# Optimization experiments

Hardware: AMD Instinct MI355X
Metric: run time of the kernel (lower is better)

Reference implementation:

```python
import jax, jax.numpy as jnp
import numpy as np
from jax import lax

NB, NC, NH, NW, NT, NCLASS = 128, 256, 8, 128, 64, 128
NHID = NC // 2  # bidirectional LSTM hidden per direction


def _lengths():
    rng = np.random.default_rng(0)
    lengths = rng.integers(NT // 2, NT + 1, size=NB)
    lengths[0] = NT  # ensure nsteps == nT
    return lengths


def setup_inputs() -> dict:
    key = jax.random.key(0)
    ks = jax.random.split(key, 20)
    s = 0.05
    lengths = _lengths()
    d = {}
    d['feature'] = jax.random.normal(ks[0], (NB, NC, NH, NW), jnp.float32)
    d['A'] = jax.random.uniform(ks[1], (NB, NT, NH, NW), jnp.float32, 1e-3, 1.0)
    d['text'] = jax.random.randint(ks[2], (NB, NT), 0, NCLASS)
    d['text_length'] = jnp.asarray(lengths, jnp.int32)
    d['pack_b'] = jnp.asarray(np.repeat(np.arange(NB), lengths), jnp.int32)
    d['pack_t'] = jnp.asarray(np.concatenate([np.arange(l) for l in lengths]), jnp.int32)
    d['emb'] = jax.random.normal(ks[3], (NCLASS, NC), jnp.float32)  # char_embeddings ~ randn
    # pre_lstm (PyTorch gate order i,f,g,o), forward and backward directions
    d['Wih_f'] = s * jax.random.normal(ks[4], (4 * NHID, NC), jnp.float32)
    d['Whh_f'] = s * jax.random.normal(ks[5], (4 * NHID, NHID), jnp.float32)
    d['bih_f'] = s * jax.random.normal(ks[6], (4 * NHID,), jnp.float32)
    d['bhh_f'] = s * jax.random.normal(ks[7], (4 * NHID,), jnp.float32)
    d['Wih_b'] = s * jax.random.normal(ks[8], (4 * NHID, NC), jnp.float32)
    d['Whh_b'] = s * jax.random.normal(ks[9], (4 * NHID, NHID), jnp.float32)
    d['bih_b'] = s * jax.random.normal(ks[10], (4 * NHID,), jnp.float32)
    d['bhh_b'] = s * jax.random.normal(ks[11], (4 * NHID,), jnp.float32)
    # GRUCell (PyTorch gate order r,z,n): input 2*NC, hidden NC
    d['Wih_g'] = s * jax.random.normal(ks[12], (3 * NC, 2 * NC), jnp.float32)
    d['Whh_g'] = s * jax.random.normal(ks[13], (3 * NC, NC), jnp.float32)
    d['bih_g'] = s * jax.random.normal(ks[14], (3 * NC,), jnp.float32)
    d['bhh_g'] = s * jax.random.normal(ks[15], (3 * NC,), jnp.float32)
    # generator Linear NC -> NCLASS (dropout treated as identity for determinism)
    d['Wgen'] = s * jax.random.normal(ks[16], (NCLASS, NC), jnp.float32)
    d['bgen'] = s * jax.random.normal(ks[17], (NCLASS,), jnp.float32)
    return d


def _lstm_dir(x, Wih, Whh, bih, bhh, reverse):
    nB = x.shape[1]
    h0 = jnp.zeros((nB, Whh.shape[1]), x.dtype)
    b = bih + bhh

    def step(carry, xt):
        h, c = carry
        g = xt @ Wih.T + h @ Whh.T + b
        i, f, gg, o = jnp.split(g, 4, axis=-1)
        c = jax.nn.sigmoid(f) * c + jax.nn.sigmoid(i) * jnp.tanh(gg)
        h = jax.nn.sigmoid(o) * jnp.tanh(c)
        return (h, c), h

    _, ys = lax.scan(step, (h0, h0), x, reverse=reverse)
    return ys


def reference(feature, A, text, text_length, pack_b, pack_t, emb, Wih_f, Whh_f, bih_f, bhh_f, Wih_b, Whh_b, bih_b, bhh_b, Wih_g, Whh_g, bih_g, bhh_g, Wgen, bgen):
    # normalize attention maps over spatial dims
    A_norm = A / A.reshape(NB, NT, -1).sum(-1)[:, :, None, None]  # [nB,nT,nH,nW]
    # attention-pooled features, fused (avoids [nB,nT,nC,nH,nW] blowup): -> [nT,nB,nC]
    C = jnp.einsum('bchw,bthw->tbc', feature, A_norm)
    # bidirectional LSTM (dropout after LSTM treated as identity)
    Cf = _lstm_dir(C, Wih_f, Whh_f, bih_f, bhh_f, False)
    Cb = _lstm_dir(C, Wih_b, Whh_b, bih_b, bhh_b, True)
    Cl = jnp.concatenate([Cf, Cb], axis=-1)  # [nT,nB,nC]
    # teacher forcing (current_epoch=0): prev_emb[0]=emb[0], prev_emb[t]=emb[text[:,t-1]]
    prev = jnp.concatenate([jnp.broadcast_to(emb[0][None, None, :], (1, NB, NC)), emb[text[:, :NT - 1].T]], axis=0)
    xs = jnp.concatenate([Cl, prev], axis=-1)  # [nT,nB,2*nC]
    h0 = jnp.zeros((NB, NC), C.dtype)

    def gstep(h, xt):
        gx = xt @ Wih_g.T + bih_g
        gh = h @ Whh_g.T + bhh_g
        rx, zx, nx = jnp.split(gx, 3, axis=-1)
        rh, zh, nh = jnp.split(gh, 3, axis=-1)
        r = jax.nn.sigmoid(rx + rh)
        z = jax.nn.sigmoid(zx + zh)
        n = jnp.tanh(nx + r * nh)
        h = (1.0 - z) * n + z * h
        return h, h

    _, hs = lax.scan(gstep, h0, xs)  # [nT,nB,nC]
    logits = hs @ Wgen.T + bgen  # [nT,nB,nclass]
    # ragged packing: concat per-sample valid steps (vectorized gather)
    out_res = logits[pack_t, pack_b]  # [lenText,nclass]
    out_attns = A_norm[pack_b, pack_t]  # [lenText,nH,nW]
    return out_res, out_attns
```

## Files before the change

kernel.cpp:

```cpp
#include <hip/hip_runtime.h>
#include <cstdint>
#include <cstddef>

#define NBATCH 128
#define NCH    256
#define NHW    1024
#define NTIME  64
#define NCLS   128

typedef _Float16 f16_t;
typedef _Float16 f16x8 __attribute__((ext_vector_type(8)));
typedef _Float16 half2_t __attribute__((ext_vector_type(2)));
typedef short bf16x8 __attribute__((ext_vector_type(8)));
typedef short bf16x4 __attribute__((ext_vector_type(4)));
typedef float f32x4 __attribute__((ext_vector_type(4)));
typedef unsigned short ushort_t;

#if defined(__has_builtin)
#  if __has_builtin(__builtin_amdgcn_fdot2)
#    define HAS_FDOT2 1
#  endif
#endif
#ifndef HAS_FDOT2
#  define HAS_FDOT2 0
#endif

__device__ __forceinline__ float dot2acc(half2_t a, half2_t b, float c){
#if HAS_FDOT2
  return __builtin_amdgcn_fdot2(a, b, c, false);
#else
  return c + (float)a.x*(float)b.x + (float)a.y*(float)b.y;
#endif
}
__device__ __forceinline__ half2_t pack2(float x, float y){
  half2_t p; p.x = (_Float16)x; p.y = (_Float16)y; return p;
}
#define BCH(x) __builtin_bit_cast(half2_t, (x))
__device__ __forceinline__ ushort_t f2bf(float x){
  unsigned u = __builtin_bit_cast(unsigned, x);
  unsigned r = (u + 0x7FFFu + ((u>>16)&1u)) >> 16;
  return (ushort_t)r;
}
__device__ __forceinline__ float sig_(float x){
  x = fminf(30.f, fmaxf(-30.f, x));
  return 1.f/(1.f+__expf(-x));
}
__device__ __forceinline__ float tanh_(float x){
  x = fminf(15.f, fmaxf(-15.f, x));
  float e = __expf(2.f*x);
  return (e-1.f)/(e+1.f);
}

__global__ __launch_bounds__(256) void k_prep(
    const float* __restrict__ Wih_f, const float* __restrict__ Wih_b,
    const float* __restrict__ Wih_g, const float* __restrict__ Wgen,
    const float* __restrict__ Whh_f, const float* __restrict__ Whh_b,
    const float* __restrict__ Whh_g, const float* __restrict__ emb,
    ushort_t* __restrict__ Wf_bf, ushort_t* __restrict__ Wb_bf,
    ushort_t* __restrict__ Wg_bf, ushort_t* __restrict__ Wgen_bf,
    f16_t* __restrict__ Whf_h, f16_t* __restrict__ Whb_h, f16_t* __restrict__ Whg_h,
    ushort_t* __restrict__ emb_bf){
  int i = blockIdx.x*256 + threadIdx.x;
  if (i < 131072){ Wf_bf[i] = f2bf(Wih_f[i]); return; }
  i -= 131072;
  if (i < 131072){ Wb_bf[i] = f2bf(Wih_b[i]); return; }
  i -= 131072;
  if (i < 393216){ Wg_bf[i] = f2bf(Wih_g[i]); return; }
  i -= 393216;
  if (i < 32768){ Wgen_bf[i] = f2bf(Wgen[i]); return; }
  i -= 32768;
  if (i < 65536){ Whf_h[i] = (f16_t)Whh_f[i]; return; }
  i -= 65536;
  if (i < 65536){ Whb_h[i] = (f16_t)Whh_b[i]; return; }
  i -= 65536;
  if (i < 196608){ Whg_h[i] = (f16_t)Whh_g[i]; return; }
  i -= 196608;
  emb_bf[i] = f2bf(emb[i]);
}

__global__ __launch_bounds__(256) void k_pool_mfma(const float* __restrict__ feat, const float* __restrict__ A,
    float* __restrict__ S, ushort_t* __restrict__ Cbf){
  __shared__ ushort_t As_[64*40];
  __shared__ ushort_t Fs_[128*40];
  __shared__ float sinvs[64];
  __shared__ float psum[512];
  int b = blockIdx.x >> 1, ch = blockIdx.x & 1, c0 = ch*128;
  int tid = threadIdx.x, wave = tid>>6, lane = tid&63;
  f32x4 acc[4][2] = {};
  int lr = lane & 15, lk = (lane>>4)*8;
  float sA0 = 0.f, sA1 = 0.f;
  for (int k0=0;k0<NHW;k0+=32){
    __syncthreads();
    #pragma unroll
    for (int i=0;i<2;i++){
      int c = tid + i*256, r = c>>3, kq = c&7;
      float4 v = *(const float4*)(A + ((size_t)(b*64+r))*NHW + k0 + kq*4);
      float sv = v.x+v.y+v.z+v.w;
      if (i==0) sA0 += sv; else sA1 += sv;
      bf16x4 p; p[0]=(short)f2bf(v.x); p[1]=(short)f2bf(v.y); p[2]=(short)f2bf(v.z); p[3]=(short)f2bf(v.w);
      *(bf16x4*)&As_[r*40 + kq*4] = p;
    }
    #pragma unroll
    for (int i=0;i<4;i++){
      int c = tid + i*256, r = c>>3, kq = c&7;
      float4 v = *(const float4*)(feat + ((size_t)(b*256+c0+r))*NHW + k0 + kq*4);
      bf16x4 p; p[0]=(short)f2bf(v.x); p[1]=(short)f2bf(v.y); p[2]=(short)f2bf(v.z); p[3]=(short)f2bf(v.w);
      *(bf16x4*)&Fs_[r*40 + kq*4] = p;
    }
    __syncthreads();
    bf16x8 af[4], bg[2];
    #pragma unroll
    for (int m=0;m<4;m++) af[m] = *(const bf16x8*)&As_[(m*16 + lr)*40 + lk];
    #pragma unroll
    for (int n=0;n<2;n++) bg[n] = *(const bf16x8*)&Fs_[(wave*32 + n*16 + lr)*40 + lk];
    #pragma unroll
    for (int m=0;m<4;m++)
      #pragma unroll
      for (int n=0;n<2;n++)
        acc[m][n] = __builtin_amdgcn_mfma_f32_16x16x32_bf16(af[m], bg[n], acc[m][n], 0, 0, 0);
  }
  psum[tid] = sA0;
  psum[tid+256] = sA1;
  __syncthreads();
  if (tid < 64){
    float s = 0.f;
    #pragma unroll
    for (int j=0;j<8;j++) s += psum[tid*8 + j];
    sinvs[tid] = 1.f / s;
    if (ch == 0) S[b*64 + tid] = s;
  }
  __syncthreads();
  #pragma unroll
  for (int m=0;m<4;m++)
    #pragma unroll
    for (int n=0;n<2;n++)
      #pragma unroll
      for (int j=0;j<4;j++){
        int t = m*16 + (lane>>4)*4 + j;
        int c = c0 + wave*32 + n*16 + lr;
        Cbf[((size_t)t*NBATCH + b)*NCH + c] = f2bf(acc[m][n][j] * sinvs[t]);
      }
}

__global__ __launch_bounds__(256) void k_gemm_bf(const ushort_t* __restrict__ X, const ushort_t* __restrict__ W,
    const float* __restrict__ ba, const float* __restrict__ bb, float* __restrict__ out, int N, int K){
  __shared__ ushort_t Xs[128*40];
  __shared__ ushort_t Ws[128*40];
  int n0 = blockIdx.x*128, m0 = blockIdx.y*128;
  int tid = threadIdx.x, wave = tid>>6, lane = tid&63;
  int wr = wave>>1, wc = wave&1;
  int lr = lane & 15, lk = (lane>>4)*8;
  f32x4 acc[4][4] = {};
  for (int k0=0;k0<K;k0+=32){
    __syncthreads();
    #pragma unroll
    for (int i=0;i<2;i++){
      int c = tid + i*256, r = c>>2, kb = c&3;
      *(bf16x8*)&Xs[r*40 + kb*8] = *(const bf16x8*)(X + (size_t)(m0+r)*K + k0 + kb*8);
      *(bf16x8*)&Ws[r*40 + kb*8] = *(const bf16x8*)(W + (size_t)(n0+r)*K + k0 + kb*8);
    }
    __syncthreads();
    bf16x8 af[4], bg[4];
    #pragma unroll
    for (int m=0;m<4;m++) af[m] = *(const bf16x8*)&Xs[(wr*64 + m*16 + lr)*40 + lk];
    #pragma unroll
    for (int n=0;n<4;n++) bg[n] = *(const bf16x8*)&Ws[(wc*64 + n*16 + lr)*40 + lk];
    #pragma unroll
    for (int m=0;m<4;m++)
      #pragma unroll
      for (int n=0;n<4;n++)
        acc[m][n] = __builtin_amdgcn_mfma_f32_16x16x32_bf16(af[m], bg[n], acc[m][n], 0, 0, 0);
  }
  float bsv[4];
  #pragma unroll
  for (int n=0;n<4;n++){
    int col = n0 + wc*64 + n*16 + lr;
    bsv[n] = ba[col] + (bb ? bb[col] : 0.f);
  }
  #pragma unroll
  for (int m=0;m<4;m++)
    #pragma unroll
    for (int n=0;n<4;n++)
      #pragma unroll
      for (int j=0;j<4;j++){
        int row = m0 + wr*64 + m*16 + (lane>>4)*4 + j;
        int col = n0 + wc*64 + n*16 + lr;
        out[(size_t)row*N + col] = acc[m][n][j] + bsv[n];
      }
}

__global__ __launch_bounds__(256) void k_gemm_gx(const ushort_t* __restrict__ Clbf,
    const ushort_t* __restrict__ emb_bf, const int* __restrict__ text,
    const ushort_t* __restrict__ W, const float* __restrict__ ba,
    float* __restrict__ out){
  __shared__ ushort_t Xs[128*40];
  __shared__ ushort_t Ws[128*40];
  __shared__ int clsL[128];
  const int N = 768, K = 512;
  int n0 = blockIdx.x*128, m0 = blockIdx.y*128;
  int tid = threadIdx.x, wave = tid>>6, lane = tid&63;
  int wr = wave>>1, wc = wave&1;
  int lr = lane & 15, lk = (lane>>4)*8;
  if (tid < 128){
    int m = m0 + tid, t = m>>7, b = m&127;
    clsL[tid] = (t==0) ? 0 : text[b*64 + (t-1)];
  }
  f32x4 acc[4][4] = {};
  __syncthreads();
  for (int k0=0;k0<K;k0+=32){
    __syncthreads();
    #pragma unroll
    for (int i=0;i<2;i++){
      int c = tid + i*256, r = c>>2, kb = c&3;
      int col = k0 + kb*8;
      bf16x8 xv;
      if (col < 256) xv = *(const bf16x8*)(Clbf + (size_t)(m0+r)*NCH + col);
      else           xv = *(const bf16x8*)(emb_bf + (size_t)clsL[r]*NCH + (col-256));
      *(bf16x8*)&Xs[r*40 + kb*8] = xv;
      *(bf16x8*)&Ws[r*40 + kb*8] = *(const bf16x8*)(W + (size_t)(n0+r)*K + k0 + kb*8);
    }
    __syncthreads();
    bf16x8 af[4], bg[4];
    #pragma unroll
    for (int m=0;m<4;m++) af[m] = *(const bf16x8*)&Xs[(wr*64 + m*16 + lr)*40 + lk];
    #pragma unroll
    for (int n=0;n<4;n++) bg[n] = *(const bf16x8*)&Ws[(wc*64 + n*16 + lr)*40 + lk];
    #pragma unroll
    for (int m=0;m<4;m++)
      #pragma unroll
      for (int n=0;n<4;n++)
        acc[m][n] = __builtin_amdgcn_mfma_f32_16x16x32_bf16(af[m], bg[n], acc[m][n], 0, 0, 0);
  }
  float bsv[4];
  #pragma unroll
  for (int n=0;n<4;n++) bsv[n] = ba[n0 + wc*64 + n*16 + lr];
  #pragma unroll
  for (int m=0;m<4;m++)
    #pragma unroll
    for (int n=0;n<4;n++)
      #pragma unroll
      for (int j=0;j<4;j++){
        int row = m0 + wr*64 + m*16 + (lane>>4)*4 + j;
        int col = n0 + wc*64 + n*16 + lr;
        out[(size_t)row*N + col] = acc[m][n][j] + bsv[n];
      }
}

__global__ __launch_bounds__(256) void k_attns(const float* __restrict__ A, const float* __restrict__ S,
    const int* __restrict__ pack_b, const int* __restrict__ pack_t, float* __restrict__ outA){
  int i = blockIdx.x;
  int b = pack_b[i], t = pack_t[i];
  float is = 1.f / S[b*64 + t];
  float4 v = ((const float4*)(A + ((size_t)(b*64+t))*NHW))[threadIdx.x];
  v.x*=is; v.y*=is; v.z*=is; v.w*=is;
  ((float4*)(outA + (size_t)i*NHW))[threadIdx.x] = v;
}

__global__ __launch_bounds__(512) void k_lstm_ldsT(const float* __restrict__ Gf, const float* __restrict__ Gb,
    const f16_t* __restrict__ Whf, const f16_t* __restrict__ Whb, ushort_t* __restrict__ Clbf){
  extern __shared__ char smem[];
  int2*  Wt2   = (int2*)smem;
  float* h32   = (float*)(smem + 131072);
  float* gates = (float*)(smem + 131072 + 512);
  int b = blockIdx.x & 127, dir = blockIdx.x >> 7;
  const f16_t* W = dir ? Whb : Whf;
  const float* G = dir ? Gb : Gf;
  int g = threadIdx.x, lane = g & 63;
  {
    const int2* wr = (const int2*)(W + (size_t)g*128);
    #pragma unroll
    for (int p2=0;p2<32;p2++) Wt2[p2*512 + g] = wr[p2];
  }
  if (g < 128) h32[g] = 0.f;
  float c = 0.f;
  __syncthreads();
  #pragma unroll 1
  for (int t=0;t<NTIME;t++){
    int tt = dir ? (NTIME-1-t) : t;
    float gv = G[((size_t)tt*NBATCH + b)*512 + g];
    float2 hp2 = *(const float2*)(h32 + 2*lane);
    int hpk = __builtin_bit_cast(int, pack2(hp2.x, hp2.y));
    float a0=0.f, a1=0.f, a2=0.f, a3=0.f;
    #pragma unroll
    for (int p2=0;p2<32;p2+=2){
      int2 w0 = Wt2[p2*512 + g];
      int2 w1 = Wt2[(p2+1)*512 + g];
      int h0 = __builtin_amdgcn_readlane(hpk, 2*p2);
      int h1 = __builtin_amdgcn_readlane(hpk, 2*p2+1);
      int h2 = __builtin_amdgcn_readlane(hpk, 2*p2+2);
      int h3 = __builtin_amdgcn_readlane(hpk, 2*p2+3);
      a0 = dot2acc(BCH(w0.x), BCH(h0), a0);
      a1 = dot2acc(BCH(w0.y), BCH(h1), a1);
      a2 = dot2acc(BCH(w1.x), BCH(h2), a2);
      a3 = dot2acc(BCH(w1.y), BCH(h3), a3);
    }
    gates[g] = gv + a0+a1+a2+a3;
    __syncthreads();
    if (g < 128){
      float gi=gates[g], gf=gates[128+g], gg=gates[256+g], go=gates[384+g];
      c = sig_(gf)*c + sig_(gi)*tanh_(gg);
      float h = sig_(go)*tanh_(c);
      h32[g] = h;
      Clbf[((size_t)tt*NBATCH + b)*NCH + dir*128 + g] = f2bf(h);
    }
    __syncthreads();
  }
}

__global__ __launch_bounds__(512, 1) void k_gru(const float* __restrict__ gx,
    const float* __restrict__ Whh_g, const float* __restrict__ bhh_g, ushort_t* __restrict__ hsbf){
  int b = blockIdx.x, t0 = threadIdx.x, lane = t0 & 63, w = t0 >> 6;
  half2_t wpA[64], wpB[64], wpC[64];
  int pidxA, pidxB, pidxC;
  int hfbA, hfbB, hfbC;

#define LOADW(WP, PIDX, HFB, S) do { \
    int c = w*3 + (S); \
    int hf = (c >= 12) ? 1 : 0; \
    int row = (c - hf*12)*64 + lane; \
    PIDX = hf*768 + row; \
    HFB  = __builtin_amdgcn_readfirstlane(hf*32); \
    const float4* wr = (const float4*)(Whh_g + (size_t)row*256 + hf*128); \
    _Pragma("unroll") \
    for (int j=0;j<32;j++){ \
      float4 v = wr[j]; \
      WP[2*j]   = pack2(v.x, v.y); \
      WP[2*j+1] = pack2(v.z, v.w); \
    } \
  } while(0)

  LOADW(wpA, pidxA, hfbA, 0);
  LOADW(wpB, pidxB, hfbB, 1);
  LOADW(wpC, pidxC, hfbC, 2);
#undef LOADW

  __shared__ float h32[256];
  __shared__ float partLds[1536];
  __shared__ float bhL[768];
  if (t0 < 256) h32[t0] = 0.f;
  bhL[t0] = bhh_g[t0];
  if (t0 < 256) bhL[512+t0] = bhh_g[512+t0];
  float hprev = 0.f;
  __syncthreads();
  #pragma unroll 1
  for (int t=0;t<NTIME;t++){
    float gxr=0.f, gxz=0.f, gxn=0.f;
    if (t0 < 256){
      const float* gxp = gx + ((size_t)t*NBATCH + b)*768;
      gxr = gxp[t0]; gxz = gxp[256+t0]; gxn = gxp[512+t0];
    }
    float4 hq = *(const float4*)(h32 + 4*lane);
    int hpk0 = __builtin_bit_cast(int, pack2(hq.x, hq.y));
    int hpk1 = __builtin_bit_cast(int, pack2(hq.z, hq.w));

#define DOTASK(WP, PIDX, HFB) do { \
    float a0=0.f, a1=0.f, a2=0.f, a3=0.f; \
    _Pragma("unroll") \
    for (int jj=0;jj<64;jj+=2){ \
      int hv0 = __builtin_amdgcn_readlane(hpk0, HFB + (jj>>1)); \
      int hv1 = __builtin_amdgcn_readlane(hpk1, HFB + (jj>>1)); \
      if ((jj>>1)&1){ \
        a2 = dot2acc(WP[jj],   __builtin_bit_cast(half2_t, hv0), a2); \
        a3 = dot2acc(WP[jj+1], __builtin_bit_cast(half2_t, hv1), a3); \
      } else { \
        a0 = dot2acc(WP[jj],   __builtin_bit_cast(half2_t, hv0), a0); \
        a1 = dot2acc(WP[jj+1], __builtin_bit_cast(half2_t, hv1), a1); \
      } \
    } \
    partLds[PIDX] = a0+a1+a2+a3; \
  } while(0)

    DOTASK(wpA, pidxA, hfbA);
    DOTASK(wpB, pidxB, hfbB);
    DOTASK(wpC, pidxC, hfbC);
#undef DOTASK

    __syncthreads();
    if (t0 < 256){
      float rh = bhL[t0]     + partLds[t0]     + partLds[768+t0];
      float zh = bhL[256+t0] + partLds[256+t0] + partLds[1024+t0];
      float nh = bhL[512+t0] + partLds[512+t0] + partLds[1280+t0];
      float r = sig_(gxr + rh);
      float z = sig_(gxz + zh);
      float n = tanh_(gxn + r*nh);
      float h = (1.f-z)*n + z*hprev;
      hprev = h;
      h32[t0] = h;
      hsbf[((size_t)t*NBATCH + b)*NCH + t0] = f2bf(h);
    }
    __syncthreads();
  }
}

__global__ __launch_bounds__(256) void k_logits_mfma(const ushort_t* __restrict__ hsbf,
    const int* __restrict__ pack_t, const int* __restrict__ pack_b,
    const ushort_t* __restrict__ Wbf, const float* __restrict__ bias,
    float* __restrict__ out, int L){
  __shared__ ushort_t Xs[64*40];
  __shared__ ushort_t Ws[128*40];
  __shared__ int rrow[64];
  int m0 = blockIdx.x*64;
  int tid = threadIdx.x, wave = tid>>6, lane = tid&63;
  int lr = lane & 15, lk = (lane>>4)*8;
  if (tid < 64){
    int m = m0 + tid;
    int pt = (m<L) ? pack_t[m] : 0;
    int pb = (m<L) ? pack_b[m] : 0;
    rrow[tid] = pt*NBATCH + pb;
  }
  f32x4 acc[4][2] = {};
  for (int k0=0;k0<NCH;k0+=32){
    __syncthreads();
    {
      int r = tid>>2, kb = tid&3;
      *(bf16x8*)&Xs[r*40 + kb*8] = *(const bf16x8*)(hsbf + (size_t)rrow[r]*NCH + k0 + kb*8);
    }
    #pragma unroll
    for (int i=0;i<2;i++){
      int c = tid + i*256, r = c>>2, kb = c&3;
      *(bf16x8*)&Ws[r*40 + kb*8] = *(const bf16x8*)(Wbf + (size_t)r*NCH + k0 + kb*8);
    }
    __syncthreads();
    bf16x8 af[4], bg[2];
    #pragma unroll
    for (int m=0;m<4;m++) af[m] = *(const bf16x8*)&Xs[(m*16 + lr)*40 + lk];
    #pragma unroll
    for (int n=0;n<2;n++) bg[n] = *(const bf16x8*)&Ws[(wave*32 + n*16 + lr)*40 + lk];
    #pragma unroll
    for (int m=0;m<4;m++)
      #pragma unroll
      for (int n=0;n<2;n++)
        acc[m][n] = __builtin_amdgcn_mfma_f32_16x16x32_bf16(af[m], bg[n], acc[m][n], 0, 0, 0);
  }
  #pragma unroll
  for (int m=0;m<4;m++)
    #pragma unroll
    for (int n=0;n<2;n++)
      #pragma unroll
      for (int j=0;j<4;j++){
        int row = m0 + m*16 + (lane>>4)*4 + j;
        int col = wave*32 + n*16 + lr;
        if (row < L) out[(size_t)row*NCLS + col] = acc[m][n][j] + bias[col];
      }
}

extern "C" void kernel_launch(void* const* d_in, const int* in_sizes, int n_in,
                              void* d_out, int out_size, void* d_ws, size_t ws_size,
                              hipStream_t stream) {
  const float* feature = (const float*)d_in[0];
  const float* A       = (const float*)d_in[1];
  const int*   text    = (const int*)d_in[2];
  const int*   pack_b  = (const int*)d_in[4];
  const int*   pack_t  = (const int*)d_in[5];
  const float* emb     = (const float*)d_in[6];
  const float* Wih_f   = (const float*)d_in[7];
  const float* Whh_f   = (const float*)d_in[8];
  const float* bih_f   = (const float*)d_in[9];
  const float* bhh_f   = (const float*)d_in[10];
  const float* Wih_b   = (const float*)d_in[11];
  const float* Whh_b   = (const float*)d_in[12];
  const float* bih_b   = (const float*)d_in[13];
  const float* bhh_b   = (const float*)d_in[14];
  const float* Wih_g   = (const float*)d_in[15];
  const float* Whh_g   = (const float*)d_in[16];
  const float* bih_g   = (const float*)d_in[17];
  const float* bhh_g   = (const float*)d_in[18];
  const float* Wgen    = (const float*)d_in[19];
  const float* bgen    = (const float*)d_in[20];
  int L = in_sizes[4];

  char* ws = (char*)d_ws;
  const size_t KB = 1024, MB = 1u<<20;
  float*    S       = (float*)(ws + 0);
  ushort_t* Wf_bf   = (ushort_t*)(ws + 1*MB);
  ushort_t* Wb_bf   = (ushort_t*)(ws + 1*MB + 256*KB);
  ushort_t* Wg_bf   = (ushort_t*)(ws + 1*MB + 512*KB);
  ushort_t* Wgen_bf = (ushort_t*)(ws + 2*MB + 256*KB);
  f16_t*    Whf_h   = (f16_t*)(ws + 2*MB + 512*KB);
  f16_t*    Whb_h   = (f16_t*)(ws + 2*MB + 640*KB);
  f16_t*    Whg_h   = (f16_t*)(ws + 2*MB + 768*KB);
  ushort_t* emb_bf  = (ushort_t*)(ws + 3*MB + 256*KB);
  ushort_t* Cbf     = (ushort_t*)(ws + 4*MB);
  ushort_t* Clbf    = (ushort_t*)(ws + 8*MB);
  ushort_t* hsbf    = (ushort_t*)(ws + 12*MB);
  float*    Gf      = (float*)(ws + 16*MB);
  float*    Gb      = (float*)(ws + 32*MB);
  float*    gx      = (float*)(ws + 24*MB);

  float* out_res   = (float*)d_out;
  float* out_attns = out_res + (size_t)L*NCLS;

  const int LSTM_SMEM = 131072 + 512 + 2048;
  (void)hipFuncSetAttribute((const void*)k_lstm_ldsT,
                            hipFuncAttributeMaxDynamicSharedMemorySize, LSTM_SMEM);

  k_prep<<<4096, 256, 0, stream>>>(Wih_f, Wih_b, Wih_g, Wgen, Whh_f, Whh_b, Whh_g, emb,
                                   Wf_bf, Wb_bf, Wg_bf, Wgen_bf, Whf_h, Whb_h, Whg_h, emb_bf);
  k_pool_mfma<<<256, 256, 0, stream>>>(feature, A, S, Cbf);
  k_attns<<<L, 256, 0, stream>>>(A, S, pack_b, pack_t, out_attns);
  k_gemm_bf<<<dim3(4,64), 256, 0, stream>>>(Cbf, Wf_bf, bih_f, bhh_f, Gf, 512, 256);
  k_gemm_bf<<<dim3(4,64), 256, 0, stream>>>(Cbf, Wb_bf, bih_b, bhh_b, Gb, 512, 256);
  k_lstm_ldsT<<<256, 512, LSTM_SMEM, stream>>>(Gf, Gb, Whf_h, Whb_h, Clbf);
  k_gemm_gx<<<dim3(6,64), 256, 0, stream>>>(Clbf, emb_bf, text, Wg_bf, bih_g, gx);
  k_gru<<<128, 512, 0, stream>>>(gx, Whh_g, bhh_g, hsbf);
  k_logits_mfma<<<(L+63)/64, 256, 0, stream>>>(hsbf, pack_t, pack_b, Wgen_bf, bgen, out_res, L);
}
```

Before: 324.8 us.

## Replicate recurrent cell update per wave to drop second barrier in LSTM and GRU

```diff
diff --git a/kernel.cpp b/kernel.cpp
--- a/kernel.cpp
+++ b/kernel.cpp
@@ -260,26 +260,24 @@
     const f16_t* __restrict__ Whf, const f16_t* __restrict__ Whb, ushort_t* __restrict__ Clbf){
   extern __shared__ char smem[];
   int2*  Wt2   = (int2*)smem;
-  float* h32   = (float*)(smem + 131072);
-  float* gates = (float*)(smem + 131072 + 512);
+  float* gates = (float*)(smem + 131072);
   int b = blockIdx.x & 127, dir = blockIdx.x >> 7;
   const f16_t* W = dir ? Whb : Whf;
   const float* G = dir ? Gb : Gf;
-  int g = threadIdx.x, lane = g & 63;
+  int g = threadIdx.x, lane = g & 63, w = g >> 6;
   {
     const int2* wr = (const int2*)(W + (size_t)g*128);
     #pragma unroll
     for (int p2=0;p2<32;p2++) Wt2[p2*512 + g] = wr[p2];
   }
-  if (g < 128) h32[g] = 0.f;
-  float c = 0.f;
+  int hpk = 0;
+  float c0s = 0.f, c1s = 0.f;
+  int buf = 0;
   __syncthreads();
   #pragma unroll 1
   for (int t=0;t<NTIME;t++){
     int tt = dir ? (NTIME-1-t) : t;
     float gv = G[((size_t)tt*NBATCH + b)*512 + g];
-    float2 hp2 = *(const float2*)(h32 + 2*lane);
-    int hpk = __builtin_bit_cast(int, pack2(hp2.x, hp2.y));
     float a0=0.f, a1=0.f, a2=0.f, a3=0.f;
     #pragma unroll
     for (int p2=0;p2<32;p2+=2){
@@ -294,16 +292,25 @@
       a2 = dot2acc(BCH(w1.x), BCH(h2), a2);
       a3 = dot2acc(BCH(w1.y), BCH(h3), a3);
     }
-    gates[g] = gv + a0+a1+a2+a3;
-    __syncthreads();
-    if (g < 128){
-      float gi=gates[g], gf=gates[128+g], gg=gates[256+g], go=gates[384+g];
-      c = sig_(gf)*c + sig_(gi)*tanh_(gg);
-      float h = sig_(go)*tanh_(c);
-      h32[g] = h;
-      Clbf[((size_t)tt*NBATCH + b)*NCH + dir*128 + g] = f2bf(h);
-    }
-    __syncthreads();
+    gates[buf*512 + g] = gv + a0+a1+a2+a3;
+    __syncthreads();
+    {
+      const float* GT = gates + buf*512;
+      float2 gi = *(const float2*)(GT + 2*lane);
+      float2 gf = *(const float2*)(GT + 128 + 2*lane);
+      float2 gg = *(const float2*)(GT + 256 + 2*lane);
+      float2 go = *(const float2*)(GT + 384 + 2*lane);
+      c0s = sig_(gf.x)*c0s + sig_(gi.x)*tanh_(gg.x);
+      float h0 = sig_(go.x)*tanh_(c0s);
+      c1s = sig_(gf.y)*c1s + sig_(gi.y)*tanh_(gg.y);
+      float h1 = sig_(go.y)*tanh_(c1s);
+      hpk = __builtin_bit_cast(int, pack2(h0, h1));
+      if (w == 0){
+        ushort2 o; o.x = f2bf(h0); o.y = f2bf(h1);
+        *(ushort2*)(Clbf + ((size_t)tt*NBATCH + b)*NCH + dir*128 + 2*lane) = o;
+      }
+    }
+    buf ^= 1;
   }
 }
 
@@ -334,24 +341,17 @@
   LOADW(wpC, pidxC, hfbC, 2);
 #undef LOADW
 
-  __shared__ float h32[256];
-  __shared__ float partLds[1536];
-  __shared__ float bhL[768];
-  if (t0 < 256) h32[t0] = 0.f;
-  bhL[t0] = bhh_g[t0];
-  if (t0 < 256) bhL[512+t0] = bhh_g[512+t0];
-  float hprev = 0.f;
+  __shared__ float partLds[2*1536];
+  float4 bR = *(const float4*)(bhh_g + 4*lane);
+  float4 bZ = *(const float4*)(bhh_g + 256 + 4*lane);
+  float4 bN = *(const float4*)(bhh_g + 512 + 4*lane);
+  float hp0=0.f, hp1=0.f, hp2=0.f, hp3=0.f;
+  int hpk0 = 0, hpk1 = 0;
+  int buf = 0;
   __syncthreads();
   #pragma unroll 1
   for (int t=0;t<NTIME;t++){
-    float gxr=0.f, gxz=0.f, gxn=0.f;
-    if (t0 < 256){
-      const float* gxp = gx + ((size_t)t*NBATCH + b)*768;
-      gxr = gxp[t0]; gxz = gxp[256+t0]; gxn = gxp[512+t0];
-    }
-    float4 hq = *(const float4*)(h32 + 4*lane);
-    int hpk0 = __builtin_bit_cast(int, pack2(hq.x, hq.y));
-    int hpk1 = __builtin_bit_cast(int, pack2(hq.z, hq.w));
+    float* P = partLds + buf*1536;
 
 #define DOTASK(WP, PIDX, HFB) do { \
     float a0=0.f, a1=0.f, a2=0.f, a3=0.f; \
@@ -367,7 +367,7 @@
         a1 = dot2acc(WP[jj+1], __builtin_bit_cast(half2_t, hv1), a1); \
       } \
     } \
-    partLds[PIDX] = a0+a1+a2+a3; \
+    P[PIDX] = a0+a1+a2+a3; \
   } while(0)
 
     DOTASK(wpA, pidxA, hfbA);
@@ -376,19 +376,38 @@
 #undef DOTASK
 
     __syncthreads();
-    if (t0 < 256){
-      float rh = bhL[t0]     + partLds[t0]     + partLds[768+t0];
-      float zh = bhL[256+t0] + partLds[256+t0] + partLds[1024+t0];
-      float nh = bhL[512+t0] + partLds[512+t0] + partLds[1280+t0];
-      float r = sig_(gxr + rh);
-      float z = sig_(gxz + zh);
-      float n = tanh_(gxn + r*nh);
-      float h = (1.f-z)*n + z*hprev;
-      hprev = h;
-      h32[t0] = h;
-      hsbf[((size_t)t*NBATCH + b)*NCH + t0] = f2bf(h);
-    }
-    __syncthreads();
+    {
+      float4 rA = *(const float4*)(P + 4*lane);
+      float4 rB = *(const float4*)(P + 768 + 4*lane);
+      float4 zA = *(const float4*)(P + 256 + 4*lane);
+      float4 zB = *(const float4*)(P + 1024 + 4*lane);
+      float4 nA = *(const float4*)(P + 512 + 4*lane);
+      float4 nB = *(const float4*)(P + 1280 + 4*lane);
+      const float* gxp = gx + ((size_t)t*NBATCH + b)*768;
+      float4 gR = *(const float4*)(gxp + 4*lane);
+      float4 gZ = *(const float4*)(gxp + 256 + 4*lane);
+      float4 gN = *(const float4*)(gxp + 512 + 4*lane);
+      float h[4];
+      #pragma unroll
+      for (int j=0;j<4;j++){
+        float rh = ((const float*)&bR)[j] + ((const float*)&rA)[j] + ((const float*)&rB)[j];
+        float zh = ((const float*)&bZ)[j] + ((const float*)&zA)[j] + ((const float*)&zB)[j];
+        float nh = ((const float*)&bN)[j] + ((const float*)&nA)[j] + ((const float*)&nB)[j];
+        float r = sig_(((const float*)&gR)[j] + rh);
+        float z = sig_(((const float*)&gZ)[j] + zh);
+        float n = tanh_(((const float*)&gN)[j] + r*nh);
+        float hp = (j==0)?hp0:(j==1)?hp1:(j==2)?hp2:hp3;
+        h[j] = (1.f - z)*n + z*hp;
+      }
+      hp0=h[0]; hp1=h[1]; hp2=h[2]; hp3=h[3];
+      hpk0 = __builtin_bit_cast(int, pack2(h[0], h[1]));
+      hpk1 = __builtin_bit_cast(int, pack2(h[2], h[3]));
+      if (w == 0){
+        ushort4 o; o.x=f2bf(h[0]); o.y=f2bf(h[1]); o.z=f2bf(h[2]); o.w=f2bf(h[3]);
+        *(ushort4*)(hsbf + ((size_t)t*NBATCH + b)*NCH + 4*lane) = o;
+      }
+    }
+    buf ^= 1;
   }
 }
 
@@ -490,7 +509,7 @@
   float* out_res   = (float*)d_out;
   float* out_attns = out_res + (size_t)L*NCLS;
 
-  const int LSTM_SMEM = 131072 + 512 + 2048;
+  const int LSTM_SMEM = 131072 + 2*512*4;
   (void)hipFuncSetAttribute((const void*)k_lstm_ldsT,
                             hipFuncAttributeMaxDynamicSharedMemorySize, LSTM_SMEM);
 
```

Result: slower. 388.9 us (+19.7%).

## Split GRU recurrent matvec across 1024 threads with four-way K split

Applied to the files above, without the earlier changes.

```diff
diff --git a/kernel.cpp b/kernel.cpp
--- a/kernel.cpp
+++ b/kernel.cpp
@@ -307,39 +307,32 @@
   }
 }
 
-__global__ __launch_bounds__(512, 1) void k_gru(const float* __restrict__ gx,
+__global__ __launch_bounds__(1024) void k_gru(const float* __restrict__ gx,
     const float* __restrict__ Whh_g, const float* __restrict__ bhh_g, ushort_t* __restrict__ hsbf){
   int b = blockIdx.x, t0 = threadIdx.x, lane = t0 & 63, w = t0 >> 6;
-  half2_t wpA[64], wpB[64], wpC[64];
-  int pidxA, pidxB, pidxC;
-  int hfbA, hfbB, hfbC;
-
-#define LOADW(WP, PIDX, HFB, S) do { \
-    int c = w*3 + (S); \
-    int hf = (c >= 12) ? 1 : 0; \
-    int row = (c - hf*12)*64 + lane; \
-    PIDX = hf*768 + row; \
-    HFB  = __builtin_amdgcn_readfirstlane(hf*32); \
-    const float4* wr = (const float4*)(Whh_g + (size_t)row*256 + hf*128); \
-    _Pragma("unroll") \
-    for (int j=0;j<32;j++){ \
-      float4 v = wr[j]; \
-      WP[2*j]   = pack2(v.x, v.y); \
-      WP[2*j+1] = pack2(v.z, v.w); \
-    } \
-  } while(0)
-
-  LOADW(wpA, pidxA, hfbA, 0);
-  LOADW(wpB, pidxB, hfbB, 1);
-  LOADW(wpC, pidxC, hfbC, 2);
-#undef LOADW
-
+  half2_t wp[3][32];
+  int pidx[3];
+  int q16[3];
+  #pragma unroll
+  for (int s=0;s<3;s++){
+    int c = w*3 + s;
+    int q = c/12, rg = c - q*12;
+    int row = rg*64 + lane;
+    pidx[s] = q*768 + row;
+    q16[s]  = __builtin_amdgcn_readfirstlane(q*16);
+    const float4* wr = (const float4*)(Whh_g + (size_t)row*256 + q*64);
+    #pragma unroll
+    for (int j=0;j<16;j++){
+      float4 v = wr[j];
+      wp[s][2*j]   = pack2(v.x, v.y);
+      wp[s][2*j+1] = pack2(v.z, v.w);
+    }
+  }
   __shared__ float h32[256];
-  __shared__ float partLds[1536];
+  __shared__ float partLds[3072];
   __shared__ float bhL[768];
   if (t0 < 256) h32[t0] = 0.f;
-  bhL[t0] = bhh_g[t0];
-  if (t0 < 256) bhL[512+t0] = bhh_g[512+t0];
+  if (t0 < 768) bhL[t0] = bhh_g[t0];
   float hprev = 0.f;
   __syncthreads();
   #pragma unroll 1
@@ -352,34 +345,27 @@
     float4 hq = *(const float4*)(h32 + 4*lane);
     int hpk0 = __builtin_bit_cast(int, pack2(hq.x, hq.y));
     int hpk1 = __builtin_bit_cast(int, pack2(hq.z, hq.w));
-
-#define DOTASK(WP, PIDX, HFB) do { \
-    float a0=0.f, a1=0.f, a2=0.f, a3=0.f; \
-    _Pragma("unroll") \
-    for (int jj=0;jj<64;jj+=2){ \
-      int hv0 = __builtin_amdgcn_readlane(hpk0, HFB + (jj>>1)); \
-      int hv1 = __builtin_amdgcn_readlane(hpk1, HFB + (jj>>1)); \
-      if ((jj>>1)&1){ \
-        a2 = dot2acc(WP[jj],   __builtin_bit_cast(half2_t, hv0), a2); \
-        a3 = dot2acc(WP[jj+1], __builtin_bit_cast(half2_t, hv1), a3); \
-      } else { \
-        a0 = dot2acc(WP[jj],   __builtin_bit_cast(half2_t, hv0), a0); \
-        a1 = dot2acc(WP[jj+1], __builtin_bit_cast(half2_t, hv1), a1); \
-      } \
-    } \
-    partLds[PIDX] = a0+a1+a2+a3; \
-  } while(0)
-
-    DOTASK(wpA, pidxA, hfbA);
-    DOTASK(wpB, pidxB, hfbB);
-    DOTASK(wpC, pidxC, hfbC);
-#undef DOTASK
-
+    #pragma unroll
+    for (int s=0;s<3;s++){
+      float a0=0.f, a1=0.f, a2=0.f, a3=0.f;
+      #pragma unroll
+      for (int u=0;u<32;u+=4){
+        int h0 = __builtin_amdgcn_readlane(hpk0, q16[s] + (u>>1));
+        int h1 = __builtin_amdgcn_readlane(hpk1, q16[s] + (u>>1));
+        int h2 = __builtin_amdgcn_readlane(hpk0, q16[s] + (u>>1) + 1);
+        int h3 = __builtin_amdgcn_readlane(hpk1, q16[s] + (u>>1) + 1);
+        a0 = dot2acc(wp[s][u],   BCH(h0), a0);
+        a1 = dot2acc(wp[s][u+1], BCH(h1), a1);
+        a2 = dot2acc(wp[s][u+2], BCH(h2), a2);
+        a3 = dot2acc(wp[s][u+3], BCH(h3), a3);
+      }
+      partLds[pidx[s]] = a0+a1+a2+a3;
+    }
     __syncthreads();
     if (t0 < 256){
-      float rh = bhL[t0]     + partLds[t0]     + partLds[768+t0];
-      float zh = bhL[256+t0] + partLds[256+t0] + partLds[1024+t0];
-      float nh = bhL[512+t0] + partLds[512+t0] + partLds[1280+t0];
+      float rh = bhL[t0]     + partLds[t0]     + partLds[768+t0]      + partLds[1536+t0]      + partLds[2304+t0];
+      float zh = bhL[256+t0] + partLds[256+t0] + partLds[768+256+t0]  + partLds[1536+256+t0]  + partLds[2304+256+t0];
+      float nh = bhL[512+t0] + partLds[512+t0] + partLds[768+512+t0]  + partLds[1536+512+t0]  + partLds[2304+512+t0];
       float r = sig_(gxr + rh);
       float z = sig_(gxz + zh);
       float n = tanh_(gxn + r*nh);
@@ -502,6 +488,6 @@
   k_gemm_bf<<<dim3(4,64), 256, 0, stream>>>(Cbf, Wb_bf, bih_b, bhh_b, Gb, 512, 256);
   k_lstm_ldsT<<<256, 512, LSTM_SMEM, stream>>>(Gf, Gb, Whf_h, Whb_h, Clbf);
   k_gemm_gx<<<dim3(6,64), 256, 0, stream>>>(Clbf, emb_bf, text, Wg_bf, bih_g, gx);
-  k_gru<<<128, 512, 0, stream>>>(gx, Whh_g, bhh_g, hsbf);
+  k_gru<<<128, 1024, 0, stream>>>(gx, Whh_g, bhh_g, hsbf);
   k_logits_mfma<<<(L+63)/64, 256, 0, stream>>>(hsbf, pack_t, pack_b, Wgen_bf, bgen, out_res, L);
 }
```

After: 397.5 us. 22.4% more time.

## Overlap attention-map normalization with GRU recurrence using extra blocks

Applied to the files above, without the earlier changes.

```diff
diff --git a/kernel.cpp b/kernel.cpp
--- a/kernel.cpp
+++ b/kernel.cpp
@@ -7,6 +7,7 @@
 #define NHW    1024
 #define NTIME  64
 #define NCLS   128
+#define NATTN  256
 
 typedef _Float16 f16_t;
 typedef _Float16 f16x8 __attribute__((ext_vector_type(8)));
@@ -246,16 +247,6 @@
       }
 }
 
-__global__ __launch_bounds__(256) void k_attns(const float* __restrict__ A, const float* __restrict__ S,
-    const int* __restrict__ pack_b, const int* __restrict__ pack_t, float* __restrict__ outA){
-  int i = blockIdx.x;
-  int b = pack_b[i], t = pack_t[i];
-  float is = 1.f / S[b*64 + t];
-  float4 v = ((const float4*)(A + ((size_t)(b*64+t))*NHW))[threadIdx.x];
-  v.x*=is; v.y*=is; v.z*=is; v.w*=is;
-  ((float4*)(outA + (size_t)i*NHW))[threadIdx.x] = v;
-}
-
 __global__ __launch_bounds__(512) void k_lstm_ldsT(const float* __restrict__ Gf, const float* __restrict__ Gb,
     const f16_t* __restrict__ Whf, const f16_t* __restrict__ Whb, ushort_t* __restrict__ Clbf){
   extern __shared__ char smem[];
@@ -308,14 +299,32 @@
 }
 
 __global__ __launch_bounds__(512, 1) void k_gru(const float* __restrict__ gx,
-    const float* __restrict__ Whh_g, const float* __restrict__ bhh_g, ushort_t* __restrict__ hsbf){
+    const float* __restrict__ Whh_g, const float* __restrict__ bhh_g, ushort_t* __restrict__ hsbf,
+    const float* __restrict__ A, const float* __restrict__ S,
+    const int* __restrict__ pack_b, const int* __restrict__ pack_t,
+    float* __restrict__ outA, int L){
   int b = blockIdx.x, t0 = threadIdx.x, lane = t0 & 63, w = t0 >> 6;
+  if (b >= NBATCH){
+    int ab = b - NBATCH;
+    int half = t0 >> 8, q = t0 & 255;
+    for (int r0 = ab*2; r0 < L; r0 += NATTN*2){
+      int r = r0 + half;
+      if (r < L){
+        int bb = pack_b[r], tt = pack_t[r];
+        float is = 1.f / S[bb*64 + tt];
+        float4 v = ((const float4*)(A + ((size_t)(bb*64+tt))*NHW))[q];
+        v.x*=is; v.y*=is; v.z*=is; v.w*=is;
+        ((float4*)(outA + (size_t)r*NHW))[q] = v;
+      }
+    }
+    return;
+  }
   half2_t wpA[64], wpB[64], wpC[64];
   int pidxA, pidxB, pidxC;
   int hfbA, hfbB, hfbC;
 
-#define LOADW(WP, PIDX, HFB, S) do { \
-    int c = w*3 + (S); \
+#define LOADW(WP, PIDX, HFB, S_) do { \
+    int c = w*3 + (S_); \
     int hf = (c >= 12) ? 1 : 0; \
     int row = (c - hf*12)*64 + lane; \
     PIDX = hf*768 + row; \
@@ -497,11 +506,11 @@
   k_prep<<<4096, 256, 0, stream>>>(Wih_f, Wih_b, Wih_g, Wgen, Whh_f, Whh_b, Whh_g, emb,
                                    Wf_bf, Wb_bf, Wg_bf, Wgen_bf, Whf_h, Whb_h, Whg_h, emb_bf);
   k_pool_mfma<<<256, 256, 0, stream>>>(feature, A, S, Cbf);
-  k_attns<<<L, 256, 0, stream>>>(A, S, pack_b, pack_t, out_attns);
   k_gemm_bf<<<dim3(4,64), 256, 0, stream>>>(Cbf, Wf_bf, bih_f, bhh_f, Gf, 512, 256);
   k_gemm_bf<<<dim3(4,64), 256, 0, stream>>>(Cbf, Wb_bf, bih_b, bhh_b, Gb, 512, 256);
   k_lstm_ldsT<<<256, 512, LSTM_SMEM, stream>>>(Gf, Gb, Whf_h, Whb_h, Clbf);
   k_gemm_gx<<<dim3(6,64), 256, 0, stream>>>(Clbf, emb_bf, text, Wg_bf, bih_g, gx);
-  k_gru<<<128, 512, 0, stream>>>(gx, Whh_g, bhh_g, hsbf);
+  k_gru<<<NBATCH + NATTN, 512, 0, stream>>>(gx, Whh_g, bhh_g, hsbf,
+                                            A, S, pack_b, pack_t, out_attns, L);
   k_logits_mfma<<<(L+63)/64, 256, 0, stream>>>(hsbf, pack_t, pack_b, Wgen_bf, bgen, out_res, L);
 }
```

After: 316.0 us. 1.03x faster.
